# Performance work log

Hardware: AMD Instinct MI355X
Metric: run time of the kernel (lower is better)

Reference implementation:

```python
import jax, jax.numpy as jnp
import numpy as np

N, E, IN_DIM, HIDDEN, OUT_DIM = 100000, 800000, 128, 128, 40
EPS = 1e-5


def setup_inputs() -> dict:
    key = jax.random.key(0)
    ks = jax.random.split(key, 20)
    x = jax.random.normal(ks[0], (N, IN_DIM), dtype=jnp.float32)
    edge_index = jax.random.randint(ks[1], (2, E), 0, N, dtype=jnp.int64)

    def lin(k, fan_in, fan_out):
        return jax.random.normal(k, (fan_in, fan_out), dtype=jnp.float32) / np.sqrt(fan_in)

    d = {"x": x, "edge_index": edge_index}
    dims = [(IN_DIM, HIDDEN), (HIDDEN, HIDDEN), (HIDDEN, HIDDEN), (HIDDEN, OUT_DIM)]
    ki = 2
    for i, (fi, fo) in enumerate(dims, start=1):
        d[f"Wl{i}"] = lin(ks[ki], fi, fo); ki += 1   # lin_l: applied to aggregated neighbors (has bias)
        d[f"bl{i}"] = jnp.zeros((fo,), jnp.float32)
        d[f"Wr{i}"] = lin(ks[ki], fi, fo); ki += 1   # lin_r: applied to root node (no bias, PyG default)
    for i in (1, 2, 3):
        d[f"g{i}"] = jnp.ones((HIDDEN,), jnp.float32)   # BatchNorm gamma
        d[f"b{i}"] = jnp.zeros((HIDDEN,), jnp.float32)  # BatchNorm beta
    return d


def _sage_conv(x, src, dst, inv_cnt, Wl, bl, Wr):
    # mean-aggregate neighbor features: gather x[src], scatter-add at dst, divide by in-degree
    agg = jax.ops.segment_sum(x[src], dst, num_segments=N) * inv_cnt  # [N, F]
    return agg @ Wl + bl + x @ Wr


def _bn(x, g, b):
    # batch-statistics normalization (training-mode BatchNorm1d, biased variance)
    mu = jnp.mean(x, axis=0)
    var = jnp.mean(jnp.square(x - mu), axis=0)
    return (x - mu) * jax.lax.rsqrt(var + EPS) * g + b


def reference(x, edge_index, Wl1, bl1, Wr1, Wl2, bl2, Wr2, Wl3, bl3, Wr3,
              Wl4, bl4, Wr4, g1, b1, g2, b2, g3, b3):
    src, dst = edge_index[0], edge_index[1]
    cnt = jax.ops.segment_sum(jnp.ones((E,), jnp.float32), dst, num_segments=N)
    inv_cnt = (1.0 / jnp.maximum(cnt, 1.0))[:, None]  # [N, 1]

    h = jax.nn.relu(_bn(_sage_conv(x, src, dst, inv_cnt, Wl1, bl1, Wr1), g1, b1))
    h = jax.nn.relu(_bn(_sage_conv(h, src, dst, inv_cnt, Wl2, bl2, Wr2), g2, b2))
    h = jax.nn.relu(_bn(_sage_conv(h, src, dst, inv_cnt, Wl3, bl3, Wr3), g3, b3))
    out = _sage_conv(h, src, dst, inv_cnt, Wl4, bl4, Wr4)
    return jax.nn.log_softmax(out, axis=1)
```

## Files before the change

kernel.cpp:

```cpp
#include <hip/hip_runtime.h>
#include <math.h>

#define NN 100000
#define NE 800000
#define F 128
#define KK 256
#define OUTD 40
#define EPSF 1e-5f
#define NB 391
#define LROWS 64
#define NLB 1563

__global__ void detect_kernel(const int* __restrict__ ei_raw, int* __restrict__ flag) {
  __shared__ int any;
  if (threadIdx.x == 0) any = 0;
  __syncthreads();
  if (ei_raw[2 * threadIdx.x + 1] != 0) atomicOr(&any, 1);
  __syncthreads();
  if (threadIdx.x == 0) *flag = (any == 0) ? 1 : 0;
}

__global__ __launch_bounds__(256) void conv_kernel(const int* __restrict__ ei_raw,
                                                   const int* __restrict__ flag,
                                                   int* __restrict__ es) {
  int i = blockIdx.x * 256 + threadIdx.x;
  if (i < 2 * NE) {
    int f = *flag;
    es[i] = f ? ei_raw[2 * i] : ei_raw[i];
  }
}

__global__ __launch_bounds__(256) void deg_kernel(const int* __restrict__ dst,
                                                  int* __restrict__ deg) {
  int e = blockIdx.x * 256 + threadIdx.x;
  if (e < NE) atomicAdd(&deg[dst[e]], 1);
}

__global__ __launch_bounds__(256) void scan1(const int* __restrict__ deg,
                                             int* __restrict__ offs,
                                             int* __restrict__ bsum) {
  __shared__ int sh[256];
  const int tid = threadIdx.x;
  const int i = blockIdx.x * 256 + tid;
  int v = (i < NN) ? deg[i] : 0;
  sh[tid] = v;
  __syncthreads();
#pragma unroll
  for (int off = 1; off < 256; off <<= 1) {
    int add = (tid >= off) ? sh[tid - off] : 0;
    __syncthreads();
    sh[tid] += add;
    __syncthreads();
  }
  if (i < NN) offs[i] = sh[tid] - v;
  if (tid == 255) bsum[blockIdx.x] = sh[255];
}

__global__ void scan2(int* __restrict__ bsum) {
  __shared__ int sh[512];
  const int t = threadIdx.x;
  int v = (t < NB) ? bsum[t] : 0;
  sh[t] = v;
  __syncthreads();
#pragma unroll
  for (int off = 1; off < 512; off <<= 1) {
    int add = (t >= off) ? sh[t - off] : 0;
    __syncthreads();
    sh[t] += add;
    __syncthreads();
  }
  if (t < NB) bsum[t] = sh[t] - v;
}

__global__ __launch_bounds__(256) void scan3(int* __restrict__ offs,
                                             int* __restrict__ woff,
                                             const int* __restrict__ bsum) {
  int i = blockIdx.x * 256 + threadIdx.x;
  if (i < NN) {
    int o = offs[i] + bsum[blockIdx.x];
    offs[i] = o;
    woff[i] = o;
  }
  if (i == 0) offs[NN] = NE;
}

__global__ __launch_bounds__(256) void fill_kernel(const int* __restrict__ src,
                                                   const int* __restrict__ dst,
                                                   int* __restrict__ woff,
                                                   int* __restrict__ eidx) {
  int e = blockIdx.x * 256 + threadIdx.x;
  if (e < NE) {
    int pos = atomicAdd(&woff[dst[e]], 1);
    eidx[pos] = src[e];
  }
}

__global__ __launch_bounds__(256) void transpose_w(const float* __restrict__ Wl,
                                                   const float* __restrict__ Wr,
                                                   float* __restrict__ Wt) {
  int i = blockIdx.x * 256 + threadIdx.x;
  if (i < OUTD * KK) {
    int j = i / KK, k = i - j * KK;
    Wt[i] = (k < F) ? Wl[k * OUTD + j] : Wr[(k - F) * OUTD + j];
  }
}

__device__ __forceinline__ void bnrelu4(float4& v, const float4& s, const float4& b) {
  v.x = fmaxf(fmaf(v.x, s.x, b.x), 0.f);
  v.y = fmaxf(fmaf(v.y, s.y, b.y), 0.f);
  v.z = fmaxf(fmaf(v.z, s.z, b.z), 0.f);
  v.w = fmaxf(fmaf(v.w, s.w, b.w), 0.f);
}

template <int BN>
__device__ __forceinline__ void gather_row(const float* __restrict__ hin,
                                           const int* __restrict__ eidx,
                                           int beg, int end, int q,
                                           const float4& scl, const float4& shf,
                                           float4& out) {
  float ax = 0.f, ay = 0.f, az = 0.f, aw = 0.f;
#define ACCV(vv)                                       \
  do {                                                 \
    if (BN) bnrelu4(vv, scl, shf);                     \
    ax += vv.x; ay += vv.y; az += vv.z; aw += vv.w;    \
  } while (0)
  int i = beg;
  for (; i + 8 <= end; i += 8) {
    int s0 = eidx[i],     s1 = eidx[i + 1], s2 = eidx[i + 2], s3 = eidx[i + 3];
    int s4 = eidx[i + 4], s5 = eidx[i + 5], s6 = eidx[i + 6], s7 = eidx[i + 7];
    float4 v0 = *(const float4*)(hin + (size_t)s0 * F + q * 4);
    float4 v1 = *(const float4*)(hin + (size_t)s1 * F + q * 4);
    float4 v2 = *(const float4*)(hin + (size_t)s2 * F + q * 4);
    float4 v3 = *(const float4*)(hin + (size_t)s3 * F + q * 4);
    float4 v4 = *(const float4*)(hin + (size_t)s4 * F + q * 4);
    float4 v5 = *(const float4*)(hin + (size_t)s5 * F + q * 4);
    float4 v6 = *(const float4*)(hin + (size_t)s6 * F + q * 4);
    float4 v7 = *(const float4*)(hin + (size_t)s7 * F + q * 4);
    ACCV(v0); ACCV(v1); ACCV(v2); ACCV(v3);
    ACCV(v4); ACCV(v5); ACCV(v6); ACCV(v7);
  }
  for (; i + 2 <= end; i += 2) {
    int s0 = eidx[i], s1 = eidx[i + 1];
    float4 v0 = *(const float4*)(hin + (size_t)s0 * F + q * 4);
    float4 v1 = *(const float4*)(hin + (size_t)s1 * F + q * 4);
    ACCV(v0); ACCV(v1);
  }
  if (i < end) {
    int s0 = eidx[i];
    float4 v0 = *(const float4*)(hin + (size_t)s0 * F + q * 4);
    ACCV(v0);
  }
#undef ACCV
  float m = 1.0f / fmaxf((float)(end - beg), 1.0f);
  out.x = ax * m; out.y = ay * m; out.z = az * m; out.w = aw * m;
}

__device__ __forceinline__ void fma_half64(const float (*tile)[F],
                                           const float* __restrict__ Wp,
                                           int tx, int ty, float acc[8][4]) {
  for (int k = 0; k < F; k += 4) {
    float4 in4[8];
#pragma unroll
    for (int r = 0; r < 8; ++r)
      in4[r] = *(const float4*)(&tile[ty * 8 + r][k]);
#pragma unroll
    for (int i = 0; i < 4; ++i) {
      float4 w = *(const float4*)(Wp + (size_t)(k + i) * F + tx * 4);
      float a[8];
#pragma unroll
      for (int r = 0; r < 8; ++r) a[r] = ((const float*)&in4[r])[i];
#pragma unroll
      for (int r = 0; r < 8; ++r) {
        acc[r][0] = fmaf(a[r], w.x, acc[r][0]);
        acc[r][1] = fmaf(a[r], w.y, acc[r][1]);
        acc[r][2] = fmaf(a[r], w.z, acc[r][2]);
        acc[r][3] = fmaf(a[r], w.w, acc[r][3]);
      }
    }
  }
}

template <int BN>
__global__ __launch_bounds__(256) void fused_layer(const float* __restrict__ hin,
                                                   const int* __restrict__ eidx,
                                                   const int* __restrict__ offs,
                                                   const float* __restrict__ sc,
                                                   const float* __restrict__ Wl,
                                                   const float* __restrict__ bl,
                                                   const float* __restrict__ Wr,
                                                   float* __restrict__ out,
                                                   float* __restrict__ sums) {
  __shared__ float tile[LROWS][F];
  const int t = threadIdx.x;
  const int row0 = blockIdx.x * LROWS;
  const int q = t & 31;
  const int grp = t >> 5;
  float4 scl, shf;
  if (BN) {
    scl = *(const float4*)(sc + q * 4);
    shf = *(const float4*)(sc + 128 + q * 4);
  }

#pragma unroll 1
  for (int rr = 0; rr < 8; ++rr) {
    int r = grp * 8 + rr;
    int n = row0 + r;
    float4 o = {0.f, 0.f, 0.f, 0.f};
    if (n < NN) {
      int beg = offs[n];
      int end = offs[n + 1];
      gather_row<BN>(hin, eidx, beg, end, q, scl, shf, o);
    }
    *(float4*)(&tile[r][q * 4]) = o;
  }

  const int tx = t & 31;
  const int ty = t >> 5;
  float acc[8][4];
#pragma unroll
  for (int r = 0; r < 8; ++r)
#pragma unroll
    for (int c = 0; c < 4; ++c) acc[r][c] = 0.f;

  fma_half64(tile, Wl, tx, ty, acc);

#pragma unroll
  for (int rr = 0; rr < 8; ++rr) {
    int r = grp * 8 + rr;
    int row = row0 + r;
    float4 v = {0.f, 0.f, 0.f, 0.f};
    if (row < NN) {
      v = *(const float4*)(hin + (size_t)row * F + q * 4);
      if (BN) bnrelu4(v, scl, shf);
    }
    *(float4*)(&tile[r][q * 4]) = v;
  }

  fma_half64(tile, Wr, tx, ty, acc);

  float4 b4 = *(const float4*)(bl + tx * 4);
  float ps[4] = {0.f, 0.f, 0.f, 0.f};
  float pq[4] = {0.f, 0.f, 0.f, 0.f};
#pragma unroll
  for (int r = 0; r < 8; ++r) {
    int row = row0 + ty * 8 + r;
    if (row < NN) {
      float4 o;
      o.x = acc[r][0] + b4.x;
      o.y = acc[r][1] + b4.y;
      o.z = acc[r][2] + b4.z;
      o.w = acc[r][3] + b4.w;
      ps[0] += o.x; pq[0] = fmaf(o.x, o.x, pq[0]);
      ps[1] += o.y; pq[1] = fmaf(o.y, o.y, pq[1]);
      ps[2] += o.z; pq[2] = fmaf(o.z, o.z, pq[2]);
      ps[3] += o.w; pq[3] = fmaf(o.w, o.w, pq[3]);
      *(float4*)(out + (size_t)row * F + tx * 4) = o;
    }
  }
  __syncthreads();
  float* red = &tile[0][0];
#pragma unroll
  for (int j = 0; j < 4; ++j) {
    red[ty * 128 + tx * 4 + j] = ps[j];
    red[2048 + ty * 128 + tx * 4 + j] = pq[j];
  }
  __syncthreads();
  if (t < 128) {
    float s = 0.f, qq = 0.f;
#pragma unroll
    for (int g2 = 0; g2 < 8; ++g2) {
      s += red[g2 * 128 + t];
      qq += red[2048 + g2 * 128 + t];
    }
    atomicAdd(&sums[t], s);
    atomicAdd(&sums[128 + t], qq);
  }
}

__global__ void bn_params(const float* __restrict__ sums, const float* __restrict__ g,
                          const float* __restrict__ b, float* __restrict__ sc) {
  int c = threadIdx.x;
  float mu = sums[c] * (1.0f / NN);
  float var = sums[128 + c] * (1.0f / NN) - mu * mu;
  float scale = g[c] * rsqrtf(var + EPSF);
  sc[c] = scale;
  sc[128 + c] = b[c] - mu * scale;
}

__global__ __launch_bounds__(256) void fused_final(const float* __restrict__ hin,
                                                   const int* __restrict__ eidx,
                                                   const int* __restrict__ offs,
                                                   const float* __restrict__ sc,
                                                   const float* __restrict__ Wt,
                                                   const float* __restrict__ bl,
                                                   float* __restrict__ out) {
  __shared__ float tile[32][F];
  const int t = threadIdx.x;
  const int row0 = blockIdx.x * 32;
  const int q = t & 31;
  const int grp = t >> 5;
  float4 scl = *(const float4*)(sc + q * 4);
  float4 shf = *(const float4*)(sc + 128 + q * 4);

#pragma unroll 1
  for (int rr = 0; rr < 4; ++rr) {
    int r = grp * 4 + rr;
    int n = row0 + r;
    int beg = offs[n];
    int end = offs[n + 1];
    float4 o;
    gather_row<1>(hin, eidx, beg, end, q, scl, shf, o);
    *(float4*)(&tile[r][q * 4]) = o;
  }

  const int tx = t & 63;
  const int wv = t >> 6;
  const int jj = (tx < OUTD) ? tx : 0;
  const float* __restrict__ wrow = Wt + (size_t)jj * KK;
  float acc[8] = {0.f, 0.f, 0.f, 0.f, 0.f, 0.f, 0.f, 0.f};
#pragma unroll 2
  for (int k = 0; k < F; k += 4) {
    float4 w = *(const float4*)(wrow + k);
#pragma unroll
    for (int r = 0; r < 8; ++r) {
      float4 a = *(const float4*)(&tile[wv * 8 + r][k]);
      acc[r] = fmaf(a.x, w.x, acc[r]);
      acc[r] = fmaf(a.y, w.y, acc[r]);
      acc[r] = fmaf(a.z, w.z, acc[r]);
      acc[r] = fmaf(a.w, w.w, acc[r]);
    }
  }

#pragma unroll
  for (int rr = 0; rr < 4; ++rr) {
    int r = grp * 4 + rr;
    float4 v = *(const float4*)(hin + (size_t)(row0 + r) * F + q * 4);
    bnrelu4(v, scl, shf);
    *(float4*)(&tile[r][q * 4]) = v;
  }

#pragma unroll 2
  for (int k = 0; k < F; k += 4) {
    float4 w = *(const float4*)(wrow + F + k);
#pragma unroll
    for (int r = 0; r < 8; ++r) {
      float4 a = *(const float4*)(&tile[wv * 8 + r][k]);
      acc[r] = fmaf(a.x, w.x, acc[r]);
      acc[r] = fmaf(a.y, w.y, acc[r]);
      acc[r] = fmaf(a.z, w.z, acc[r]);
      acc[r] = fmaf(a.w, w.w, acc[r]);
    }
  }

  float bias = bl[jj];
#pragma unroll
  for (int r = 0; r < 8; ++r) {
    float v = acc[r] + bias;
    float m = (tx < OUTD) ? v : -INFINITY;
#pragma unroll
    for (int off = 32; off > 0; off >>= 1) m = fmaxf(m, __shfl_xor(m, off));
    float e = (tx < OUTD) ? expf(v - m) : 0.f;
    float s = e;
#pragma unroll
    for (int off = 32; off > 0; off >>= 1) s += __shfl_xor(s, off);
    if (tx < OUTD) out[(size_t)(row0 + wv * 8 + r) * OUTD + tx] = v - m - logf(s);
  }
}

extern "C" void kernel_launch(void* const* d_in, const int* in_sizes, int n_in,
                              void* d_out, int out_size, void* d_ws, size_t ws_size,
                              hipStream_t stream) {
  const float* x = (const float*)d_in[0];
  const int* ei_raw = (const int*)d_in[1];
  const float* Wl[4] = {(const float*)d_in[2], (const float*)d_in[5],
                        (const float*)d_in[8], (const float*)d_in[11]};
  const float* bl[4] = {(const float*)d_in[3], (const float*)d_in[6],
                        (const float*)d_in[9], (const float*)d_in[12]};
  const float* Wr[4] = {(const float*)d_in[4], (const float*)d_in[7],
                        (const float*)d_in[10], (const float*)d_in[13]};
  const float* g[3] = {(const float*)d_in[14], (const float*)d_in[16],
                       (const float*)d_in[18]};
  const float* bb[3] = {(const float*)d_in[15], (const float*)d_in[17],
                        (const float*)d_in[19]};

  char* wsb = (char*)d_ws;
  float* hA  = (float*)wsb;                       wsb += (size_t)NN * F * 4;
  float* hB  = (float*)wsb;                       wsb += (size_t)NN * F * 4;
  int* es    = (int*)wsb;                         wsb += (size_t)2 * NE * 4;
  int* eidx  = (int*)wsb;                         wsb += (size_t)NE * 4;
  int* offs  = (int*)wsb;                         wsb += (size_t)(NN + 64) * 4;
  int* woff  = (int*)wsb;                         wsb += (size_t)(NN + 64) * 4;
  int* bsum  = (int*)wsb;                         wsb += 512 * 4;
  float* sums = (float*)wsb;                      wsb += 256 * 4;
  float* sc   = (float*)wsb;                      wsb += 256 * 4;
  float* Wt   = (float*)wsb;                      wsb += (size_t)OUTD * KK * 4;
  int* flag   = (int*)wsb;                        wsb += 256;

  int* esrc = es;
  int* edst = es + NE;

  detect_kernel<<<1, 256, 0, stream>>>(ei_raw, flag);
  conv_kernel<<<(2 * NE + 255) / 256, 256, 0, stream>>>(ei_raw, flag, es);

  hipMemsetAsync(woff, 0, NN * sizeof(int), stream);
  deg_kernel<<<NE / 256, 256, 0, stream>>>(edst, woff);
  scan1<<<NB, 256, 0, stream>>>(woff, offs, bsum);
  scan2<<<1, 512, 0, stream>>>(bsum);
  scan3<<<NB, 256, 0, stream>>>(offs, woff, bsum);
  fill_kernel<<<NE / 256, 256, 0, stream>>>(esrc, edst, woff, eidx);
  transpose_w<<<(OUTD * KK + 255) / 256, 256, 0, stream>>>(Wl[3], Wr[3], Wt);

  const float* cur = x;
  float* bufs[2] = {hA, hB};
  for (int L = 0; L < 3; ++L) {
    float* hpre = bufs[L & 1];
    hipMemsetAsync(sums, 0, 256 * sizeof(float), stream);
    if (L == 0)
      fused_layer<0><<<NLB, 256, 0, stream>>>(cur, eidx, offs, nullptr, Wl[L],
                                              bl[L], Wr[L], hpre, sums);
    else
      fused_layer<1><<<NLB, 256, 0, stream>>>(cur, eidx, offs, sc, Wl[L], bl[L],
                                              Wr[L], hpre, sums);
    bn_params<<<1, 128, 0, stream>>>(sums, g[L], bb[L], sc);
    cur = hpre;
  }
  fused_final<<<NN / 32, 256, 0, stream>>>(cur, eidx, offs, sc, Wt, bl[3],
                                           (float*)d_out);
}
```

Before: 815.5 us.

## Gather neighbor features from fp16 shadow copies to halve gather bandwidth

Adds fp16 shadow copies of the input features and of each layer's pre-activation output, and makes the neighbor gather read these half-precision rows instead of fp32. The random-access neighbor gather, which reads about 8 rows per node, is meant to move half as many bytes. In exchange it adds a conversion pass over x, an extra fp16 store per layer, and rounding error in the aggregated features. It also drops the 2-wide tail unroll in the gather loop.

```diff
diff --git a/kernel.cpp b/kernel.cpp
--- a/kernel.cpp
+++ b/kernel.cpp
@@ -1,4 +1,5 @@
 #include <hip/hip_runtime.h>
+#include <hip/hip_fp16.h>
 #include <math.h>
 
 #define NN 100000
@@ -11,6 +12,31 @@
 #define LROWS 64
 #define NLB 1563
 
+union H4 {
+  ushort4 u;
+  _Float16 h[4];
+};
+
+__device__ __forceinline__ float4 ld_h4(const ushort* p) {
+  H4 a;
+  a.u = *(const ushort4*)p;
+  float4 f;
+  f.x = (float)a.h[0];
+  f.y = (float)a.h[1];
+  f.z = (float)a.h[2];
+  f.w = (float)a.h[3];
+  return f;
+}
+
+__device__ __forceinline__ ushort4 st_h4(const float4& v) {
+  H4 a;
+  a.h[0] = (_Float16)v.x;
+  a.h[1] = (_Float16)v.y;
+  a.h[2] = (_Float16)v.z;
+  a.h[3] = (_Float16)v.w;
+  return a.u;
+}
+
 __global__ void detect_kernel(const int* __restrict__ ei_raw, int* __restrict__ flag) {
   __shared__ int any;
   if (threadIdx.x == 0) any = 0;
@@ -27,6 +53,15 @@
   if (i < 2 * NE) {
     int f = *flag;
     es[i] = f ? ei_raw[2 * i] : ei_raw[i];
+  }
+}
+
+__global__ __launch_bounds__(256) void conv_x(const float* __restrict__ x,
+                                              ushort* __restrict__ xh) {
+  int i = blockIdx.x * 256 + threadIdx.x;
+  if (i < NN * F / 4) {
+    float4 v = *(const float4*)(x + (size_t)i * 4);
+    *(ushort4*)(xh + (size_t)i * 4) = st_h4(v);
   }
 }
 
@@ -113,44 +148,42 @@
 }
 
 template <int BN>
-__device__ __forceinline__ void gather_row(const float* __restrict__ hin,
+__device__ __forceinline__ void gather_row(const ushort* __restrict__ hinh,
                                            const int* __restrict__ eidx,
                                            int beg, int end, int q,
                                            const float4& scl, const float4& shf,
                                            float4& out) {
   float ax = 0.f, ay = 0.f, az = 0.f, aw = 0.f;
-#define ACCV(vv)                                       \
-  do {                                                 \
-    if (BN) bnrelu4(vv, scl, shf);                     \
-    ax += vv.x; ay += vv.y; az += vv.z; aw += vv.w;    \
-  } while (0)
   int i = beg;
   for (; i + 8 <= end; i += 8) {
     int s0 = eidx[i],     s1 = eidx[i + 1], s2 = eidx[i + 2], s3 = eidx[i + 3];
     int s4 = eidx[i + 4], s5 = eidx[i + 5], s6 = eidx[i + 6], s7 = eidx[i + 7];
-    float4 v0 = *(const float4*)(hin + (size_t)s0 * F + q * 4);
-    float4 v1 = *(const float4*)(hin + (size_t)s1 * F + q * 4);
-    float4 v2 = *(const float4*)(hin + (size_t)s2 * F + q * 4);
-    float4 v3 = *(const float4*)(hin + (size_t)s3 * F + q * 4);
-    float4 v4 = *(const float4*)(hin + (size_t)s4 * F + q * 4);
-    float4 v5 = *(const float4*)(hin + (size_t)s5 * F + q * 4);
-    float4 v6 = *(const float4*)(hin + (size_t)s6 * F + q * 4);
-    float4 v7 = *(const float4*)(hin + (size_t)s7 * F + q * 4);
-    ACCV(v0); ACCV(v1); ACCV(v2); ACCV(v3);
-    ACCV(v4); ACCV(v5); ACCV(v6); ACCV(v7);
-  }
-  for (; i + 2 <= end; i += 2) {
-    int s0 = eidx[i], s1 = eidx[i + 1];
-    float4 v0 = *(const float4*)(hin + (size_t)s0 * F + q * 4);
-    float4 v1 = *(const float4*)(hin + (size_t)s1 * F + q * 4);
-    ACCV(v0); ACCV(v1);
-  }
-  if (i < end) {
+    ushort4 w0 = *(const ushort4*)(hinh + (size_t)s0 * F + q * 4);
+    ushort4 w1 = *(const ushort4*)(hinh + (size_t)s1 * F + q * 4);
+    ushort4 w2 = *(const ushort4*)(hinh + (size_t)s2 * F + q * 4);
+    ushort4 w3 = *(const ushort4*)(hinh + (size_t)s3 * F + q * 4);
+    ushort4 w4 = *(const ushort4*)(hinh + (size_t)s4 * F + q * 4);
+    ushort4 w5 = *(const ushort4*)(hinh + (size_t)s5 * F + q * 4);
+    ushort4 w6 = *(const ushort4*)(hinh + (size_t)s6 * F + q * 4);
+    ushort4 w7 = *(const ushort4*)(hinh + (size_t)s7 * F + q * 4);
+#define ACCU(ww)                                       \
+  do {                                                 \
+    H4 a_; a_.u = ww;                                  \
+    float4 vv;                                         \
+    vv.x = (float)a_.h[0]; vv.y = (float)a_.h[1];      \
+    vv.z = (float)a_.h[2]; vv.w = (float)a_.h[3];      \
+    if (BN) bnrelu4(vv, scl, shf);                     \
+    ax += vv.x; ay += vv.y; az += vv.z; aw += vv.w;    \
+  } while (0)
+    ACCU(w0); ACCU(w1); ACCU(w2); ACCU(w3);
+    ACCU(w4); ACCU(w5); ACCU(w6); ACCU(w7);
+  }
+  for (; i < end; ++i) {
     int s0 = eidx[i];
-    float4 v0 = *(const float4*)(hin + (size_t)s0 * F + q * 4);
-    ACCV(v0);
-  }
-#undef ACCV
+    ushort4 w0 = *(const ushort4*)(hinh + (size_t)s0 * F + q * 4);
+    ACCU(w0);
+  }
+#undef ACCU
   float m = 1.0f / fmaxf((float)(end - beg), 1.0f);
   out.x = ax * m; out.y = ay * m; out.z = az * m; out.w = aw * m;
 }
@@ -182,6 +215,7 @@
 
 template <int BN>
 __global__ __launch_bounds__(256) void fused_layer(const float* __restrict__ hin,
+                                                   const ushort* __restrict__ hinh,
                                                    const int* __restrict__ eidx,
                                                    const int* __restrict__ offs,
                                                    const float* __restrict__ sc,
@@ -189,6 +223,7 @@
                                                    const float* __restrict__ bl,
                                                    const float* __restrict__ Wr,
                                                    float* __restrict__ out,
+                                                   ushort* __restrict__ outh,
                                                    float* __restrict__ sums) {
   __shared__ float tile[LROWS][F];
   const int t = threadIdx.x;
@@ -209,7 +244,7 @@
     if (n < NN) {
       int beg = offs[n];
       int end = offs[n + 1];
-      gather_row<BN>(hin, eidx, beg, end, q, scl, shf, o);
+      gather_row<BN>(hinh, eidx, beg, end, q, scl, shf, o);
     }
     *(float4*)(&tile[r][q * 4]) = o;
   }
@@ -255,6 +290,7 @@
       ps[2] += o.z; pq[2] = fmaf(o.z, o.z, pq[2]);
       ps[3] += o.w; pq[3] = fmaf(o.w, o.w, pq[3]);
       *(float4*)(out + (size_t)row * F + tx * 4) = o;
+      *(ushort4*)(outh + (size_t)row * F + tx * 4) = st_h4(o);
     }
   }
   __syncthreads();
@@ -288,6 +324,7 @@
 }
 
 __global__ __launch_bounds__(256) void fused_final(const float* __restrict__ hin,
+                                                   const ushort* __restrict__ hinh,
                                                    const int* __restrict__ eidx,
                                                    const int* __restrict__ offs,
                                                    const float* __restrict__ sc,
@@ -309,7 +346,7 @@
     int beg = offs[n];
     int end = offs[n + 1];
     float4 o;
-    gather_row<1>(hin, eidx, beg, end, q, scl, shf, o);
+    gather_row<1>(hinh, eidx, beg, end, q, scl, shf, o);
     *(float4*)(&tile[r][q * 4]) = o;
   }
 
@@ -384,8 +421,11 @@
                         (const float*)d_in[19]};
 
   char* wsb = (char*)d_ws;
-  float* hA  = (float*)wsb;                       wsb += (size_t)NN * F * 4;
-  float* hB  = (float*)wsb;                       wsb += (size_t)NN * F * 4;
+  float* hA   = (float*)wsb;                      wsb += (size_t)NN * F * 4;
+  float* hB   = (float*)wsb;                      wsb += (size_t)NN * F * 4;
+  ushort* xh  = (ushort*)wsb;                     wsb += (size_t)NN * F * 2;
+  ushort* hAh = (ushort*)wsb;                     wsb += (size_t)NN * F * 2;
+  ushort* hBh = (ushort*)wsb;                     wsb += (size_t)NN * F * 2;
   int* es    = (int*)wsb;                         wsb += (size_t)2 * NE * 4;
   int* eidx  = (int*)wsb;                         wsb += (size_t)NE * 4;
   int* offs  = (int*)wsb;                         wsb += (size_t)(NN + 64) * 4;
@@ -401,6 +441,7 @@
 
   detect_kernel<<<1, 256, 0, stream>>>(ei_raw, flag);
   conv_kernel<<<(2 * NE + 255) / 256, 256, 0, stream>>>(ei_raw, flag, es);
+  conv_x<<<(NN * F / 4 + 255) / 256, 256, 0, stream>>>(x, xh);
 
   hipMemsetAsync(woff, 0, NN * sizeof(int), stream);
   deg_kernel<<<NE / 256, 256, 0, stream>>>(edst, woff);
@@ -411,19 +452,23 @@
   transpose_w<<<(OUTD * KK + 255) / 256, 256, 0, stream>>>(Wl[3], Wr[3], Wt);
 
   const float* cur = x;
+  const ushort* curh = xh;
   float* bufs[2] = {hA, hB};
+  ushort* bufsh[2] = {hAh, hBh};
   for (int L = 0; L < 3; ++L) {
     float* hpre = bufs[L & 1];
+    ushort* hpreh = bufsh[L & 1];
     hipMemsetAsync(sums, 0, 256 * sizeof(float), stream);
     if (L == 0)
-      fused_layer<0><<<NLB, 256, 0, stream>>>(cur, eidx, offs, nullptr, Wl[L],
-                                              bl[L], Wr[L], hpre, sums);
+      fused_layer<0><<<NLB, 256, 0, stream>>>(cur, curh, eidx, offs, nullptr, Wl[L],
+                                              bl[L], Wr[L], hpre, hpreh, sums);
     else
-      fused_layer<1><<<NLB, 256, 0, stream>>>(cur, eidx, offs, sc, Wl[L], bl[L],
-                                              Wr[L], hpre, sums);
+      fused_layer<1><<<NLB, 256, 0, stream>>>(cur, curh, eidx, offs, sc, Wl[L], bl[L],
+                                              Wr[L], hpre, hpreh, sums);
     bn_params<<<1, 128, 0, stream>>>(sums, g[L], bb[L], sc);
     cur = hpre;
-  }
-  fused_final<<<NN / 32, 256, 0, stream>>>(cur, eidx, offs, sc, Wt, bl[3],
+    curh = hpreh;
+  }
+  fused_final<<<NN / 32, 256, 0, stream>>>(cur, curh, eidx, offs, sc, Wt, bl[3],
                                            (float*)d_out);
 }
```

Result: slower. 839.4 us (+2.9%).
